# Performance work log

Hardware: AMD Instinct MI355X
Metric: run time of the kernel (lower is better)

The kernel has to match this reference:

```python
import jax, jax.numpy as jnp
import numpy as np

N, E = 50000, 800000
INF, ONF, HNF = 64, 64, 128
EPS = 1e-8


def qmul(p, q):
    # roma XYZW Hamilton product
    px, py, pz, pw = p[:, 0], p[:, 1], p[:, 2], p[:, 3]
    qx, qy, qz, qw = q[:, 0], q[:, 1], q[:, 2], q[:, 3]
    return jnp.stack([
        pw * qx + px * qw + py * qz - pz * qy,
        pw * qy - px * qz + py * qw + pz * qx,
        pw * qz + px * qy - py * qx + pz * qw,
        pw * qw - px * qx - py * qy - pz * qz,
    ], axis=1)


def qinv(q):
    conj = jnp.concatenate([-q[:, :3], q[:, 3:]], axis=1)
    return conj / jnp.sum(q * q, axis=1, keepdims=True)


def rot_apply(q, v):
    # rotate v by unit quaternion q (XYZW)
    qv, w = q[:, :3], q[:, 3:4]
    t = 2.0 * jnp.cross(qv, v)
    return v + w * t + jnp.cross(qv, t)


def quat_exponential(im):
    r = jnp.linalg.norm(im, axis=1, keepdims=True)
    u = im / r
    return jnp.concatenate([u * jnp.sin(r), jnp.cos(r)], axis=1)


def seg_sum(data, ids, n):
    return jax.ops.segment_sum(data, ids, num_segments=n)


def seg_mean(data, ids, n):
    s = seg_sum(data, ids, n)
    c = seg_sum(jnp.ones_like(data), ids, n)
    return s / jnp.maximum(c, 1.0)


def setup_inputs() -> dict:
    key = jax.random.key(0)
    ks = jax.random.split(key, 24)
    h = jax.random.normal(ks[0], (N, INF), jnp.float32)
    coord = jax.random.normal(ks[1], (N, 3), jnp.float32)
    q = jax.random.normal(ks[2], (N, 4), jnp.float32)
    quat = q / jnp.linalg.norm(q, axis=1, keepdims=True)
    edge_index = jax.random.randint(ks[3], (2, E), 0, N)

    def lin(k, fi, fo, scale=None):
        s = (1.0 / np.sqrt(fi)) if scale is None else scale
        return jax.random.uniform(k, (fi, fo), jnp.float32, -s, s)

    ein = 2 * INF + 8  # source, target, radial(1), quat_prod(4), unit_vecs(3)
    params = dict(
        We1=lin(ks[4], ein, HNF), be1=jnp.zeros((HNF,), jnp.float32),
        We2=lin(ks[5], HNF, HNF), be2=jnp.zeros((HNF,), jnp.float32),
        Wn1=lin(ks[6], HNF + INF, HNF), bn1=jnp.zeros((HNF,), jnp.float32),
        Wn2=lin(ks[7], HNF, ONF), bn2=jnp.zeros((ONF,), jnp.float32),
        Wc1=lin(ks[8], HNF, HNF), bc1=jnp.zeros((HNF,), jnp.float32),
        wc2=lin(ks[9], HNF, 1, scale=0.001),  # xavier gain 0.001, no bias
        Wq1=lin(ks[10], HNF, HNF), bq1=jnp.zeros((HNF,), jnp.float32),
        Wq2=lin(ks[11], HNF, 3), bq2=jnp.zeros((3,), jnp.float32),
    )
    return dict(h=h, edge_index=edge_index, coord=coord, quat=quat, **params)


def reference(h, edge_index, coord, quat,
              We1, be1, We2, be2, Wn1, bn1, Wn2, bn2,
              Wc1, bc1, wc2, Wq1, bq1, Wq2, bq2):
    silu = jax.nn.silu
    row, col = edge_index[0], edge_index[1]

    # invariants
    coord_diff = coord[row] - coord[col]                       # [E,3]
    qi = qinv(quat)
    quat_prod = qmul(qi[row], quat[col])                       # [E,4]
    radial = jnp.sum(coord_diff ** 2, axis=1, keepdims=True)   # [E,1]
    norm = jnp.sqrt(radial) + EPS
    unit_vecs = -rot_apply(qi[row], coord_diff / norm)         # [E,3]

    # edge model
    ein = jnp.concatenate([h[row], h[col], radial, quat_prod, unit_vecs], axis=1)
    edge_feat = silu(silu(ein @ We1 + be1) @ We2 + be2)        # [E,HNF]

    # coord model (mean agg)
    trans = coord_diff * (silu(edge_feat @ Wc1 + bc1) @ wc2)   # [E,3]
    coord = coord + seg_mean(trans, row, N)

    # quat model (mean agg)
    tan_vecs = silu(edge_feat @ Wq1 + bq1) @ Wq2 + bq2         # [E,3]
    rots = quat_exponential(seg_mean(tan_vecs, row, N))
    quat = qmul(quat, rots)

    # node model (sum agg), residual
    agg = seg_sum(edge_feat, row, N)
    nin = jnp.concatenate([h, agg], axis=1)
    h = h + (silu(nin @ Wn1 + bn1) @ Wn2 + bn2)
    return (h, coord, quat)
```

## Files before the change

### kernel.cpp

```cpp
#include <hip/hip_runtime.h>
#include <hip/hip_bf16.h>
#include <math.h>


#define N_NODES 50000
#define N_EDGES 800000
#define ASTR 172
#define NSTR 204

typedef __attribute__((ext_vector_type(4))) float f32x4;
typedef __attribute__((ext_vector_type(8))) short bf16x8;
typedef __attribute__((ext_vector_type(4))) unsigned short u16x4;
typedef __attribute__((ext_vector_type(8))) unsigned short u16x8;

static __device__ __forceinline__ unsigned short f2bf(float f) {
  return __builtin_bit_cast(unsigned short, __float2bfloat16(f));
}
static __device__ __forceinline__ float bf2f(unsigned short s) {
  unsigned int u = ((unsigned int)s) << 16;
  return __builtin_bit_cast(float, u);
}
static __device__ __forceinline__ float silu_f(float x) {
  return x * __builtin_amdgcn_rcpf(1.0f + __expf(-x));
}
static __device__ __forceinline__ void atomic_pk_add_bf16(unsigned int* addr,
                                                          float lo, float hi) {
  const unsigned int pk = ((unsigned int)f2bf(hi) << 16) | (unsigned int)f2bf(lo);
  asm volatile("global_atomic_pk_add_bf16 %0, %1, off"
               :: "v"((unsigned long long)(uintptr_t)addr), "v"(pk)
               : "memory");
}

static __device__ __forceinline__ void swz_do(const float* __restrict__ src,
                                              unsigned short* __restrict__ dst,
                                              int K, int NOUT, int NCT, int idx) {
  int lane = idx & 63, blk = idx >> 6;
  int ct = blk % NCT, kt = blk / NCT;
  int col = ct * 16 + (lane & 15);
  int kb = kt * 32 + (lane >> 4) * 8;
  u16x8 o;
  #pragma unroll
  for (int j = 0; j < 8; ++j) {
    int k = kb + j;
    o[j] = (k < K) ? f2bf(src[(size_t)k * NOUT + col]) : (unsigned short)0;
  }
  *(u16x8*)(dst + (size_t)idx * 8) = o;
}

__global__ __launch_bounds__(256) void prep1_kernel(
    const float* __restrict__ We1, const float* __restrict__ We2,
    const float* __restrict__ Wc1, const float* __restrict__ Wq1,
    const float* __restrict__ Wn1, const float* __restrict__ Wn2,
    unsigned short* __restrict__ We1b, unsigned short* __restrict__ We2b,
    unsigned short* __restrict__ Wc1b, unsigned short* __restrict__ Wq1b,
    unsigned short* __restrict__ Wn1b, unsigned short* __restrict__ Wn2b,
    const int* __restrict__ ei, int* __restrict__ cursor)
{
  const int b = blockIdx.x, t = threadIdx.x;
  if (b >= 50) {
    const int e = (b - 50) * 256 + t;
    if (e < N_EDGES) atomicAdd(&cursor[ei[e]], 1);
    return;
  }
  if (b < 10)       swz_do(We1, We1b, 136, 128, 8, b*256 + t);
  else if (b < 18)  swz_do(We2, We2b, 128, 128, 8, (b-10)*256 + t);
  else if (b < 26)  swz_do(Wc1, Wc1b, 128, 128, 8, (b-18)*256 + t);
  else if (b < 34)  swz_do(Wq1, Wq1b, 128, 128, 8, (b-26)*256 + t);
  else if (b < 46) { int i = (b-34)*256 + t; if (i < 3072) swz_do(Wn1, Wn1b, 192, 128, 8, i); }
  else              swz_do(Wn2, Wn2b, 128, 64, 4, (b-46)*256 + t);
}

__global__ void scan_kernel(int* __restrict__ cursor) {
  __shared__ int s[1024];
  const int t = threadIdx.x;
  const int C = 49;
  const int base = t * C;
  int sum = 0;
  for (int i = 0; i < C; ++i) {
    int n = base + i;
    if (n < N_NODES) sum += cursor[n];
  }
  s[t] = sum;
  __syncthreads();
  for (int d = 1; d < 1024; d <<= 1) {
    int v = (t >= d) ? s[t - d] : 0;
    __syncthreads();
    s[t] += v;
    __syncthreads();
  }
  int run = s[t] - sum;
  for (int i = 0; i < C; ++i) {
    int n = base + i;
    if (n < N_NODES) {
      int d = cursor[n];
      cursor[n] = run;
      run += d;
    }
  }
}

__global__ void scatter_kernel(const int* __restrict__ ei, int* __restrict__ cursor,
                               int2* __restrict__ rc2) {
  int e = blockIdx.x * blockDim.x + threadIdx.x;
  if (e < N_EDGES) {
    int r = ei[e];
    int pos = atomicAdd(&cursor[r], 1);
    int2 v; v.x = r; v.y = ei[N_EDGES + e];
    rc2[pos] = v;
  }
}

template <int KT, int NCT>
static __device__ __forceinline__ void mmW2(const unsigned short* __restrict__ a0,
                                            const unsigned short* __restrict__ a1,
                                            int lk,
                                            const unsigned short* __restrict__ Wb,
                                            int lane, f32x4* acc0, f32x4* acc1) {
  const f32x4 zero = {0.f, 0.f, 0.f, 0.f};
  #pragma unroll
  for (int ct = 0; ct < NCT; ++ct) { acc0[ct] = zero; acc1[ct] = zero; }
  __builtin_amdgcn_s_setprio(1);
  #pragma unroll
  for (int kt = 0; kt < KT; ++kt) {
    bf16x8 x0 = *(const bf16x8*)(a0 + kt*32 + lk*8);
    bf16x8 x1 = *(const bf16x8*)(a1 + kt*32 + lk*8);
    const u16x8* bb = (const u16x8*)Wb + (size_t)(kt*NCT)*64 + lane;
    #pragma unroll
    for (int ct = 0; ct < NCT; ++ct) {
      bf16x8 w = *(const bf16x8*)(bb + (size_t)ct*64);
      acc0[ct] = __builtin_amdgcn_mfma_f32_16x16x32_bf16(w, x0, acc0[ct], 0, 0, 0);
      acc1[ct] = __builtin_amdgcn_mfma_f32_16x16x32_bf16(w, x1, acc1[ct], 0, 0, 0);
    }
  }
  __builtin_amdgcn_s_setprio(0);
}

__global__ __launch_bounds__(128, 3) void edge_kernel(
    const float* __restrict__ h,
    const float* __restrict__ coord, const float* __restrict__ quat,
    const int2* __restrict__ rc2,
    const unsigned short* __restrict__ We1b, const unsigned short* __restrict__ We2b,
    const unsigned short* __restrict__ Wc1b, const unsigned short* __restrict__ Wq1b,
    const float* __restrict__ be1, const float* __restrict__ be2,
    const float* __restrict__ bc1, const float* __restrict__ wc2,
    const float* __restrict__ bq1, const float* __restrict__ Wq2,
    const float* __restrict__ bq2,
    unsigned int* __restrict__ agg32, float* __restrict__ transS,
    float* __restrict__ tanS, float* __restrict__ cnt)
{
  __shared__ __align__(16) unsigned short AF[64 * ASTR];

  const int tid = threadIdx.x;
  const int wv = tid >> 6, lane = tid & 63;
  const int lr = lane & 15, lk = lane >> 4;
  const int row0 = wv*32 + lr, row1 = row0 + 16;

  const int xcd = blockIdx.x & 7, idx = blockIdx.x >> 3;
  const int q = 1562, rem = 4;
  const int bid = (xcd < rem ? xcd*(q+1) : rem*(q+1) + (xcd-rem)*q) + idx;
  const int e0 = bid * 64;

  const int2 p0v = rc2[e0 + row0];
  const int2 p1v = rc2[e0 + row1];
  const int r0 = p0v.x, c0 = p0v.y, r1 = p1v.x, c1 = p1v.y;

  {
    const float* hs0 = h + (size_t)(lk < 2 ? r0 : c0) * 64 + (lk & 1) * 32;
    const float* hs1 = h + (size_t)(lk < 2 ? r1 : c1) * 64 + (lk & 1) * 32;
    const int cb = lk * 32;
    #pragma unroll
    for (int j = 0; j < 32; j += 4) {
      f32x4 v0 = *(const f32x4*)(hs0 + j);
      f32x4 v1 = *(const f32x4*)(hs1 + j);
      u16x4 q0, q1;
      #pragma unroll
      for (int i = 0; i < 4; ++i) { q0[i] = f2bf(v0[i]); q1[i] = f2bf(v1[i]); }
      *(u16x4*)&AF[row0*ASTR + cb + j] = q0;
      *(u16x4*)&AF[row1*ASTR + cb + j] = q1;
    }
  }
  const float cdx0 = coord[r0*3+0] - coord[c0*3+0];
  const float cdy0 = coord[r0*3+1] - coord[c0*3+1];
  const float cdz0 = coord[r0*3+2] - coord[c0*3+2];
  const float cdx1 = coord[r1*3+0] - coord[c1*3+0];
  const float cdy1 = coord[r1*3+1] - coord[c1*3+1];
  const float cdz1 = coord[r1*3+2] - coord[c1*3+2];
  if (lk < 2) {
    const int gr = lk ? r1 : r0, gc = lk ? c1 : c0, grow = lk ? row1 : row0;
    const float gx = lk ? cdx1 : cdx0, gy = lk ? cdy1 : cdy0, gz = lk ? cdz1 : cdz0;
    const float radial = gx*gx + gy*gy + gz*gz;
    const float nrm = sqrtf(radial) + 1e-8f;
    const f32x4 qr4 = *(const f32x4*)&quat[gr*4];
    const f32x4 qc4 = *(const f32x4*)&quat[gc*4];
    const float qix = -qr4[0], qiy = -qr4[1], qiz = -qr4[2], qiw = qr4[3];
    const float qcx = qc4[0], qcy = qc4[1], qcz = qc4[2], qcw = qc4[3];
    const float qpx = qiw*qcx + qix*qcw + qiy*qcz - qiz*qcy;
    const float qpy = qiw*qcy - qix*qcz + qiy*qcw + qiz*qcx;
    const float qpz = qiw*qcz + qix*qcy - qiy*qcx + qiz*qcw;
    const float qpw = qiw*qcw - qix*qcx - qiy*qcy - qiz*qcz;
    const float rinv = __builtin_amdgcn_rcpf(nrm);
    const float vx = gx*rinv, vy = gy*rinv, vz = gz*rinv;
    const float tx = 2.f*(qiy*vz - qiz*vy);
    const float ty = 2.f*(qiz*vx - qix*vz);
    const float tz = 2.f*(qix*vy - qiy*vx);
    const float ux = -(vx + qiw*tx + (qiy*tz - qiz*ty));
    const float uy = -(vy + qiw*ty + (qiz*tx - qix*tz));
    const float uz = -(vz + qiw*tz + (qix*ty - qiy*tx));
    u16x4 f0, f1;
    f0[0] = f2bf(radial); f0[1] = f2bf(qpx); f0[2] = f2bf(qpy); f0[3] = f2bf(qpz);
    f1[0] = f2bf(qpw);    f1[1] = f2bf(ux);  f1[2] = f2bf(uy);  f1[3] = f2bf(uz);
    *(u16x4*)&AF[grow*ASTR + 128] = f0;
    *(u16x4*)&AF[grow*ASTR + 132] = f1;
    const u16x4 z4 = {0, 0, 0, 0};
    #pragma unroll
    for (int j = 136; j < 160; j += 4) *(u16x4*)&AF[grow*ASTR + j] = z4;
  }

  f32x4 acc0[8], acc1[8];

  mmW2<5,8>(AF + row0*ASTR, AF + row1*ASTR, lk, We1b, lane, acc0, acc1);
  #pragma unroll
  for (int ct = 0; ct < 8; ++ct) {
    const int ocb = ct*16 + lk*4;
    const f32x4 b4 = *(const f32x4*)&be1[ocb];
    u16x4 k0, k1;
    #pragma unroll
    for (int i = 0; i < 4; ++i) {
      k0[i] = f2bf(silu_f(acc0[ct][i] + b4[i]));
      k1[i] = f2bf(silu_f(acc1[ct][i] + b4[i]));
    }
    *(u16x4*)&AF[row0*ASTR + ocb] = k0;
    *(u16x4*)&AF[row1*ASTR + ocb] = k1;
  }

  mmW2<4,8>(AF + row0*ASTR, AF + row1*ASTR, lk, We2b, lane, acc0, acc1);
  #pragma unroll
  for (int ct = 0; ct < 8; ++ct) {
    const int ocb = ct*16 + lk*4;
    const f32x4 b4 = *(const f32x4*)&be2[ocb];
    u16x4 k0, k1;
    #pragma unroll
    for (int i = 0; i < 4; ++i) {
      k0[i] = f2bf(silu_f(acc0[ct][i] + b4[i]));
      k1[i] = f2bf(silu_f(acc1[ct][i] + b4[i]));
    }
    *(u16x4*)&AF[row0*ASTR + ocb] = k0;
    *(u16x4*)&AF[row1*ASTR + ocb] = k1;
  }

  float pcs0 = 0.f, pcs1 = 0.f;
  mmW2<4,8>(AF + row0*ASTR, AF + row1*ASTR, lk, Wc1b, lane, acc0, acc1);
  #pragma unroll
  for (int ct = 0; ct < 8; ++ct) {
    const int ocb = ct*16 + lk*4;
    const f32x4 b4 = *(const f32x4*)&bc1[ocb];
    const f32x4 w4 = *(const f32x4*)&wc2[ocb];
    #pragma unroll
    for (int i = 0; i < 4; ++i) {
      pcs0 += silu_f(acc0[ct][i] + b4[i]) * w4[i];
      pcs1 += silu_f(acc1[ct][i] + b4[i]) * w4[i];
    }
  }
  pcs0 += __shfl_xor(pcs0, 16);  pcs0 += __shfl_xor(pcs0, 32);
  pcs1 += __shfl_xor(pcs1, 16);  pcs1 += __shfl_xor(pcs1, 32);

  float p00 = 0.f, p10 = 0.f, p20 = 0.f;
  float p01 = 0.f, p11 = 0.f, p21 = 0.f;
  mmW2<4,8>(AF + row0*ASTR, AF + row1*ASTR, lk, Wq1b, lane, acc0, acc1);
  #pragma unroll
  for (int ct = 0; ct < 8; ++ct) {
    const int ocb = ct*16 + lk*4;
    const f32x4 b4 = *(const f32x4*)&bq1[ocb];
    const float* wq = &Wq2[ocb*3];
    const f32x4 qa = *(const f32x4*)(wq);
    const f32x4 qb = *(const f32x4*)(wq + 4);
    const f32x4 qc = *(const f32x4*)(wq + 8);
    {
      const float v0 = silu_f(acc0[ct][0] + b4[0]);
      const float v1 = silu_f(acc0[ct][1] + b4[1]);
      const float v2 = silu_f(acc0[ct][2] + b4[2]);
      const float v3 = silu_f(acc0[ct][3] + b4[3]);
      p00 += v0*qa[0] + v1*qa[3] + v2*qb[2] + v3*qc[1];
      p10 += v0*qa[1] + v1*qb[0] + v2*qb[3] + v3*qc[2];
      p20 += v0*qa[2] + v1*qb[1] + v2*qc[0] + v3*qc[3];
    }
    {
      const float v0 = silu_f(acc1[ct][0] + b4[0]);
      const float v1 = silu_f(acc1[ct][1] + b4[1]);
      const float v2 = silu_f(acc1[ct][2] + b4[2]);
      const float v3 = silu_f(acc1[ct][3] + b4[3]);
      p01 += v0*qa[0] + v1*qa[3] + v2*qb[2] + v3*qc[1];
      p11 += v0*qa[1] + v1*qb[0] + v2*qb[3] + v3*qc[2];
      p21 += v0*qa[2] + v1*qb[1] + v2*qc[0] + v3*qc[3];
    }
  }
  p00 += __shfl_xor(p00, 16);  p00 += __shfl_xor(p00, 32);
  p10 += __shfl_xor(p10, 16);  p10 += __shfl_xor(p10, 32);
  p20 += __shfl_xor(p20, 16);  p20 += __shfl_xor(p20, 32);
  p01 += __shfl_xor(p01, 16);  p01 += __shfl_xor(p01, 32);
  p11 += __shfl_xor(p11, 16);  p11 += __shfl_xor(p11, 32);
  p21 += __shfl_xor(p21, 16);  p21 += __shfl_xor(p21, 32);

  #pragma unroll
  for (int g = 0; g < 2; ++g) {
    const int rg = g ? r1 : r0;
    const int rUp = __shfl_up(rg, 1, 16);
    const int rDn = __shfl_down(rg, 1, 16);
    const bool head = (lr == 0) || (rUp != rg);
    const bool tail = (lr == 15) || (rDn != rg);
    float v1, v2;
    if (lk == 3) { v1 = 1.0f; v2 = 0.f; }
    else {
      const float cdj = (lk == 0) ? (g ? cdx1 : cdx0)
                      : (lk == 1) ? (g ? cdy1 : cdy0) : (g ? cdz1 : cdz0);
      const float pj  = (lk == 0) ? (g ? p01 : p00)
                      : (lk == 1) ? (g ? p11 : p10) : (g ? p21 : p20);
      v1 = cdj * (g ? pcs1 : pcs0);
      v2 = pj + bq2[lk];
    }
    int f = head ? 1 : 0;
    #pragma unroll
    for (int d = 1; d < 16; d <<= 1) {
      const float o1 = __shfl_up(v1, d, 16);
      const float o2 = __shfl_up(v2, d, 16);
      const int   of = __shfl_up(f,  d, 16);
      if (lr >= d) {
        if (!f) { v1 += o1; v2 += o2; }
        f |= of;
      }
    }
    if (tail) {
      if (lk == 3) {
        atomicAdd(&cnt[rg], v1);
      } else {
        atomicAdd(&transS[rg*3 + lk], v1);
        atomicAdd(&tanS[rg*3 + lk], v2);
      }
    }
  }

  {
    float rl_ = 0.f, rh_ = 0.f;
    int prev = __builtin_amdgcn_readlane(r0, 0);
    #pragma unroll
    for (int k2 = 0; k2 < 32; ++k2) {
      const int rr = (k2 < 16) ? __builtin_amdgcn_readlane(r0, k2)
                               : __builtin_amdgcn_readlane(r1, k2 - 16);
      if (rr != prev) {
        atomic_pk_add_bf16(&agg32[(size_t)prev*64 + lane], rl_, rh_);
        rl_ = 0.f; rh_ = 0.f; prev = rr;
      }
      const unsigned int u = *(const unsigned int*)&AF[(wv*32 + k2)*ASTR + 2*lane];
      rl_ += bf2f((unsigned short)(u & 0xffffu));
      rh_ += bf2f((unsigned short)(u >> 16));
    }
    atomic_pk_add_bf16(&agg32[(size_t)prev*64 + lane], rl_, rh_);
  }
}

__global__ __launch_bounds__(256, 4) void node_kernel(
    const float* __restrict__ h, const float* __restrict__ coord,
    const float* __restrict__ quat,
    const unsigned short* __restrict__ aggb, const float* __restrict__ transS,
    const float* __restrict__ tanS, const float* __restrict__ cnt,
    const unsigned short* __restrict__ Wn1b, const unsigned short* __restrict__ Wn2b,
    const float* __restrict__ bn1, const float* __restrict__ bn2,
    float* __restrict__ out_h, float* __restrict__ out_c, float* __restrict__ out_q)
{
  __shared__ unsigned short A_[64][NSTR];
  const int tid = threadIdx.x;
  const int n0 = blockIdx.x * 64;

  {
    const int row = tid >> 2, sub = tid & 3;
    const int n = n0 + row;
    if (n < N_NODES) {
      if (sub < 2) {
        const float* hp = h + (size_t)n*64 + sub*32;
        #pragma unroll
        for (int j = 0; j < 32; j += 4) {
          f32x4 v = *(const f32x4*)(hp + j);
          u16x4 p;
          p[0] = f2bf(v[0]); p[1] = f2bf(v[1]); p[2] = f2bf(v[2]); p[3] = f2bf(v[3]);
          *(u16x4*)&A_[row][sub*32 + j] = p;
        }
      } else {
        const unsigned short* ap = aggb + (size_t)n*128 + (sub - 2)*64;
        #pragma unroll
        for (int j = 0; j < 64; j += 8)
          *(u16x8*)&A_[row][64 + (sub - 2)*64 + j] = *(const u16x8*)(ap + j);
      }
    } else {
      const u16x4 z4 = {0, 0, 0, 0};
      if (sub < 2) {
        #pragma unroll
        for (int j = 0; j < 32; j += 4) *(u16x4*)&A_[row][sub*32 + j] = z4;
      } else {
        #pragma unroll
        for (int j = 0; j < 64; j += 4) *(u16x4*)&A_[row][64 + (sub - 2)*64 + j] = z4;
      }
    }
  }
  __syncthreads();

  const int wv = tid >> 6, lane = tid & 63;
  const int lr = lane & 15, lk = lane >> 4;
  const int nrow = wv*16 + lr;
  f32x4 acc[8];

  {
    const f32x4 zero = {0.f, 0.f, 0.f, 0.f};
    #pragma unroll
    for (int ct = 0; ct < 8; ++ct) acc[ct] = zero;
    #pragma unroll
    for (int kt = 0; kt < 6; ++kt) {
      bf16x8 act = *(const bf16x8*)&A_[nrow][kt*32 + lk*8];
      const u16x8* bb = (const u16x8*)Wn1b + (size_t)(kt*8)*64 + lane;
      #pragma unroll
      for (int ct = 0; ct < 8; ++ct) {
        bf16x8 w = *(const bf16x8*)(bb + (size_t)ct*64);
        acc[ct] = __builtin_amdgcn_mfma_f32_16x16x32_bf16(w, act, acc[ct], 0, 0, 0);
      }
    }
  }
  #pragma unroll
  for (int ct = 0; ct < 8; ++ct) {
    const int ocb = ct*16 + lk*4;
    const f32x4 b4 = *(const f32x4*)&bn1[ocb];
    u16x4 pk;
    #pragma unroll
    for (int i = 0; i < 4; ++i) pk[i] = f2bf(silu_f(acc[ct][i] + b4[i]));
    *(u16x4*)&A_[nrow][ocb] = pk;
  }

  f32x4 acc2[4];
  {
    const f32x4 zero = {0.f, 0.f, 0.f, 0.f};
    #pragma unroll
    for (int ct = 0; ct < 4; ++ct) acc2[ct] = zero;
    #pragma unroll
    for (int kt = 0; kt < 4; ++kt) {
      bf16x8 act = *(const bf16x8*)&A_[nrow][kt*32 + lk*8];
      const u16x8* bb = (const u16x8*)Wn2b + (size_t)(kt*4)*64 + lane;
      #pragma unroll
      for (int ct = 0; ct < 4; ++ct) {
        bf16x8 w = *(const bf16x8*)(bb + (size_t)ct*64);
        acc2[ct] = __builtin_amdgcn_mfma_f32_16x16x32_bf16(w, act, acc2[ct], 0, 0, 0);
      }
    }
  }
  const int n = n0 + nrow;
  if (n < N_NODES) {
    #pragma unroll
    for (int ct = 0; ct < 4; ++ct) {
      const int ocb = ct*16 + lk*4;
      const f32x4 b4 = *(const f32x4*)&bn2[ocb];
      const f32x4 h4 = *(const f32x4*)&h[(size_t)n*64 + ocb];
      f32x4 o;
      #pragma unroll
      for (int i = 0; i < 4; ++i) o[i] = h4[i] + acc2[ct][i] + b4[i];
      *(f32x4*)&out_h[(size_t)n*64 + ocb] = o;
    }
  }

  if (tid < 64) {
    const int nn = n0 + tid;
    if (nn < N_NODES) {
      const float cm = fmaxf(cnt[nn], 1.0f);
      const float inv = 1.0f / cm;
      out_c[nn*3+0] = coord[nn*3+0] + transS[nn*3+0]*inv;
      out_c[nn*3+1] = coord[nn*3+1] + transS[nn*3+1]*inv;
      out_c[nn*3+2] = coord[nn*3+2] + transS[nn*3+2]*inv;
      const float ix = tanS[nn*3+0]*inv, iy = tanS[nn*3+1]*inv, iz = tanS[nn*3+2]*inv;
      const float rr = sqrtf(ix*ix + iy*iy + iz*iz);
      const float s = sinf(rr) / rr;
      const float rx = ix*s, ry = iy*s, rz = iz*s, rw = cosf(rr);
      const float px = quat[nn*4+0], py = quat[nn*4+1], pz = quat[nn*4+2], pw = quat[nn*4+3];
      out_q[nn*4+0] = pw*rx + px*rw + py*rz - pz*ry;
      out_q[nn*4+1] = pw*ry - px*rz + py*rw + pz*rx;
      out_q[nn*4+2] = pw*rz + px*ry - py*rx + pz*rw;
      out_q[nn*4+3] = pw*rw - px*rx - py*ry - pz*rz;
    }
  }
}

extern "C" void kernel_launch(void* const* d_in, const int* in_sizes, int n_in,
                              void* d_out, int out_size, void* d_ws, size_t ws_size,
                              hipStream_t stream) {
  (void)in_sizes; (void)n_in; (void)out_size; (void)ws_size;
  const float* h     = (const float*)d_in[0];
  const int*   ei    = (const int*)d_in[1];
  const float* coord = (const float*)d_in[2];
  const float* quat  = (const float*)d_in[3];
  const float* We1 = (const float*)d_in[4];  const float* be1 = (const float*)d_in[5];
  const float* We2 = (const float*)d_in[6];  const float* be2 = (const float*)d_in[7];
  const float* Wn1 = (const float*)d_in[8];  const float* bn1 = (const float*)d_in[9];
  const float* Wn2 = (const float*)d_in[10]; const float* bn2 = (const float*)d_in[11];
  const float* Wc1 = (const float*)d_in[12]; const float* bc1 = (const float*)d_in[13];
  const float* wc2 = (const float*)d_in[14];
  const float* Wq1 = (const float*)d_in[15]; const float* bq1 = (const float*)d_in[16];
  const float* Wq2 = (const float*)d_in[17]; const float* bq2 = (const float*)d_in[18];

  char* ws = (char*)d_ws;
  unsigned int* agg32  = (unsigned int*)(ws);
  unsigned short* aggb = (unsigned short*)(ws);
  float* transS = (float*)(ws + 12800000);
  float* tanS   = (float*)(ws + 13400000);
  float* cnt    = (float*)(ws + 14000000);
  int*   cursor = (int*)  (ws + 14200000);
  int2*  rc2    = (int2*) (ws + 14600064);
  unsigned short* We1b = (unsigned short*)(ws + 21000064);
  unsigned short* We2b = We1b + 5*8*64*8;
  unsigned short* Wc1b = We2b + 4*8*64*8;
  unsigned short* Wq1b = Wc1b + 4*8*64*8;
  unsigned short* Wn1b = Wq1b + 4*8*64*8;
  unsigned short* Wn2b = Wn1b + 6*8*64*8;

  hipMemsetAsync(ws, 0, 14400000, stream);
  prep1_kernel<<<50 + (N_EDGES + 255)/256, 256, 0, stream>>>(
      We1, We2, Wc1, Wq1, Wn1, Wn2, We1b, We2b, Wc1b, Wq1b, Wn1b, Wn2b,
      ei, cursor);
  scan_kernel<<<1, 1024, 0, stream>>>(cursor);
  scatter_kernel<<<(N_EDGES + 255)/256, 256, 0, stream>>>(ei, cursor, rc2);

  edge_kernel<<<N_EDGES/64, 128, 0, stream>>>(
      h, coord, quat, rc2, We1b, We2b, Wc1b, Wq1b,
      be1, be2, bc1, wc2, bq1, Wq2, bq2, agg32, transS, tanS, cnt);

  float* out_h = (float*)d_out;
  float* out_c = out_h + (size_t)N_NODES*64;
  float* out_q = out_c + (size_t)N_NODES*3;
  node_kernel<<<(N_NODES + 63)/64, 256, 0, stream>>>(
      h, coord, quat, aggb, transS, tanS, cnt, Wn1b, Wn2b, bn1, bn2,
      out_h, out_c, out_q);
}
```

Before: 477.2 us.

## Pre-convert h to bf16, fold biases into MFMA init, derive degree from CSR

The prep kernel now converts h to bf16 once, and both the edge and node kernels gather those bf16 rows. This halves the bytes read by the per-edge random gathers and removes the repeated per-edge conversion. The prep kernel also zeroes the aggregation buffers, so the large memset shrinks to clearing only the cursor array. Biases are loaded into the MFMA accumulators at the start instead of being added later. The per-edge count atomics are dropped, and the node kernel computes each node's degree from the CSR cursor offsets instead. The cost is an extra pass over h and more blocks in the prep launch.

```diff
diff --git a/kernel.cpp b/kernel.cpp
--- a/kernel.cpp
+++ b/kernel.cpp
@@ -51,23 +51,42 @@
     const float* __restrict__ We1, const float* __restrict__ We2,
     const float* __restrict__ Wc1, const float* __restrict__ Wq1,
     const float* __restrict__ Wn1, const float* __restrict__ Wn2,
+    const float* __restrict__ h,
     unsigned short* __restrict__ We1b, unsigned short* __restrict__ We2b,
     unsigned short* __restrict__ Wc1b, unsigned short* __restrict__ Wq1b,
     unsigned short* __restrict__ Wn1b, unsigned short* __restrict__ Wn2b,
+    unsigned short* __restrict__ hb, uint4* __restrict__ zbase,
     const int* __restrict__ ei, int* __restrict__ cursor)
 {
   const int b = blockIdx.x, t = threadIdx.x;
-  if (b >= 50) {
-    const int e = (b - 50) * 256 + t;
-    if (e < N_EDGES) atomicAdd(&cursor[ei[e]], 1);
+  if (b < 50) {
+    if (b < 10)       swz_do(We1, We1b, 136, 128, 8, b*256 + t);
+    else if (b < 18)  swz_do(We2, We2b, 128, 128, 8, (b-10)*256 + t);
+    else if (b < 26)  swz_do(Wc1, Wc1b, 128, 128, 8, (b-18)*256 + t);
+    else if (b < 34)  swz_do(Wq1, Wq1b, 128, 128, 8, (b-26)*256 + t);
+    else if (b < 46) { int i = (b-34)*256 + t; if (i < 3072) swz_do(Wn1, Wn1b, 192, 128, 8, i); }
+    else              swz_do(Wn2, Wn2b, 128, 64, 4, (b-46)*256 + t);
     return;
   }
-  if (b < 10)       swz_do(We1, We1b, 136, 128, 8, b*256 + t);
-  else if (b < 18)  swz_do(We2, We2b, 128, 128, 8, (b-10)*256 + t);
-  else if (b < 26)  swz_do(Wc1, Wc1b, 128, 128, 8, (b-18)*256 + t);
-  else if (b < 34)  swz_do(Wq1, Wq1b, 128, 128, 8, (b-26)*256 + t);
-  else if (b < 46) { int i = (b-34)*256 + t; if (i < 3072) swz_do(Wn1, Wn1b, 192, 128, 8, i); }
-  else              swz_do(Wn2, Wn2b, 128, 64, 4, (b-46)*256 + t);
+  if (b < 1613) {
+    const int i8 = (b - 50) * 2048 + t * 8;
+    if (i8 < N_NODES * 64) {
+      f32x4 v0 = *(const f32x4*)(h + i8);
+      f32x4 v1 = *(const f32x4*)(h + i8 + 4);
+      u16x8 o;
+      #pragma unroll
+      for (int i = 0; i < 4; ++i) { o[i] = f2bf(v0[i]); o[i+4] = f2bf(v1[i]); }
+      *(u16x8*)(hb + i8) = o;
+    }
+    return;
+  }
+  if (b < 5031) {
+    const int i = (b - 1613) * 256 + t;
+    if (i < 875000) { uint4 z; z.x = z.y = z.z = z.w = 0u; zbase[i] = z; }
+    return;
+  }
+  const int e = (b - 5031) * 256 + t;
+  if (e < N_EDGES) atomicAdd(&cursor[ei[e]], 1);
 }
 
 __global__ void scan_kernel(int* __restrict__ cursor) {
@@ -115,10 +134,13 @@
                                             const unsigned short* __restrict__ a1,
                                             int lk,
                                             const unsigned short* __restrict__ Wb,
+                                            const float* __restrict__ bias,
                                             int lane, f32x4* acc0, f32x4* acc1) {
-  const f32x4 zero = {0.f, 0.f, 0.f, 0.f};
-  #pragma unroll
-  for (int ct = 0; ct < NCT; ++ct) { acc0[ct] = zero; acc1[ct] = zero; }
+  #pragma unroll
+  for (int ct = 0; ct < NCT; ++ct) {
+    const f32x4 b = *(const f32x4*)&bias[ct*16 + lk*4];
+    acc0[ct] = b; acc1[ct] = b;
+  }
   __builtin_amdgcn_s_setprio(1);
   #pragma unroll
   for (int kt = 0; kt < KT; ++kt) {
@@ -136,7 +158,7 @@
 }
 
 __global__ __launch_bounds__(128, 3) void edge_kernel(
-    const float* __restrict__ h,
+    const unsigned short* __restrict__ hb,
     const float* __restrict__ coord, const float* __restrict__ quat,
     const int2* __restrict__ rc2,
     const unsigned short* __restrict__ We1b, const unsigned short* __restrict__ We2b,
@@ -146,7 +168,7 @@
     const float* __restrict__ bq1, const float* __restrict__ Wq2,
     const float* __restrict__ bq2,
     unsigned int* __restrict__ agg32, float* __restrict__ transS,
-    float* __restrict__ tanS, float* __restrict__ cnt)
+    float* __restrict__ tanS)
 {
   __shared__ __align__(16) unsigned short AF[64 * ASTR];
 
@@ -165,18 +187,13 @@
   const int r0 = p0v.x, c0 = p0v.y, r1 = p1v.x, c1 = p1v.y;
 
   {
-    const float* hs0 = h + (size_t)(lk < 2 ? r0 : c0) * 64 + (lk & 1) * 32;
-    const float* hs1 = h + (size_t)(lk < 2 ? r1 : c1) * 64 + (lk & 1) * 32;
+    const unsigned short* hs0 = hb + (size_t)(lk < 2 ? r0 : c0) * 64 + (lk & 1) * 32;
+    const unsigned short* hs1 = hb + (size_t)(lk < 2 ? r1 : c1) * 64 + (lk & 1) * 32;
     const int cb = lk * 32;
     #pragma unroll
     for (int j = 0; j < 32; j += 4) {
-      f32x4 v0 = *(const f32x4*)(hs0 + j);
-      f32x4 v1 = *(const f32x4*)(hs1 + j);
-      u16x4 q0, q1;
-      #pragma unroll
-      for (int i = 0; i < 4; ++i) { q0[i] = f2bf(v0[i]); q1[i] = f2bf(v1[i]); }
-      *(u16x4*)&AF[row0*ASTR + cb + j] = q0;
-      *(u16x4*)&AF[row1*ASTR + cb + j] = q1;
+      *(u16x4*)&AF[row0*ASTR + cb + j] = *(const u16x4*)(hs0 + j);
+      *(u16x4*)&AF[row1*ASTR + cb + j] = *(const u16x4*)(hs1 + j);
     }
   }
   const float cdx0 = coord[r0*3+0] - coord[c0*3+0];
@@ -218,47 +235,44 @@
 
   f32x4 acc0[8], acc1[8];
 
-  mmW2<5,8>(AF + row0*ASTR, AF + row1*ASTR, lk, We1b, lane, acc0, acc1);
+  mmW2<5,8>(AF + row0*ASTR, AF + row1*ASTR, lk, We1b, be1, lane, acc0, acc1);
   #pragma unroll
   for (int ct = 0; ct < 8; ++ct) {
     const int ocb = ct*16 + lk*4;
-    const f32x4 b4 = *(const f32x4*)&be1[ocb];
     u16x4 k0, k1;
     #pragma unroll
     for (int i = 0; i < 4; ++i) {
-      k0[i] = f2bf(silu_f(acc0[ct][i] + b4[i]));
-      k1[i] = f2bf(silu_f(acc1[ct][i] + b4[i]));
+      k0[i] = f2bf(silu_f(acc0[ct][i]));
+      k1[i] = f2bf(silu_f(acc1[ct][i]));
     }
     *(u16x4*)&AF[row0*ASTR + ocb] = k0;
     *(u16x4*)&AF[row1*ASTR + ocb] = k1;
   }
 
-  mmW2<4,8>(AF + row0*ASTR, AF + row1*ASTR, lk, We2b, lane, acc0, acc1);
+  mmW2<4,8>(AF + row0*ASTR, AF + row1*ASTR, lk, We2b, be2, lane, acc0, acc1);
   #pragma unroll
   for (int ct = 0; ct < 8; ++ct) {
     const int ocb = ct*16 + lk*4;
-    const f32x4 b4 = *(const f32x4*)&be2[ocb];
     u16x4 k0, k1;
     #pragma unroll
     for (int i = 0; i < 4; ++i) {
-      k0[i] = f2bf(silu_f(acc0[ct][i] + b4[i]));
-      k1[i] = f2bf(silu_f(acc1[ct][i] + b4[i]));
+      k0[i] = f2bf(silu_f(acc0[ct][i]));
+      k1[i] = f2bf(silu_f(acc1[ct][i]));
     }
     *(u16x4*)&AF[row0*ASTR + ocb] = k0;
     *(u16x4*)&AF[row1*ASTR + ocb] = k1;
   }
 
   float pcs0 = 0.f, pcs1 = 0.f;
-  mmW2<4,8>(AF + row0*ASTR, AF + row1*ASTR, lk, Wc1b, lane, acc0, acc1);
+  mmW2<4,8>(AF + row0*ASTR, AF + row1*ASTR, lk, Wc1b, bc1, lane, acc0, acc1);
   #pragma unroll
   for (int ct = 0; ct < 8; ++ct) {
     const int ocb = ct*16 + lk*4;
-    const f32x4 b4 = *(const f32x4*)&bc1[ocb];
     const f32x4 w4 = *(const f32x4*)&wc2[ocb];
     #pragma unroll
     for (int i = 0; i < 4; ++i) {
-      pcs0 += silu_f(acc0[ct][i] + b4[i]) * w4[i];
-      pcs1 += silu_f(acc1[ct][i] + b4[i]) * w4[i];
+      pcs0 += silu_f(acc0[ct][i]) * w4[i];
+      pcs1 += silu_f(acc1[ct][i]) * w4[i];
     }
   }
   pcs0 += __shfl_xor(pcs0, 16);  pcs0 += __shfl_xor(pcs0, 32);
@@ -266,29 +280,28 @@
 
   float p00 = 0.f, p10 = 0.f, p20 = 0.f;
   float p01 = 0.f, p11 = 0.f, p21 = 0.f;
-  mmW2<4,8>(AF + row0*ASTR, AF + row1*ASTR, lk, Wq1b, lane, acc0, acc1);
+  mmW2<4,8>(AF + row0*ASTR, AF + row1*ASTR, lk, Wq1b, bq1, lane, acc0, acc1);
   #pragma unroll
   for (int ct = 0; ct < 8; ++ct) {
     const int ocb = ct*16 + lk*4;
-    const f32x4 b4 = *(const f32x4*)&bq1[ocb];
     const float* wq = &Wq2[ocb*3];
     const f32x4 qa = *(const f32x4*)(wq);
     const f32x4 qb = *(const f32x4*)(wq + 4);
     const f32x4 qc = *(const f32x4*)(wq + 8);
     {
-      const float v0 = silu_f(acc0[ct][0] + b4[0]);
-      const float v1 = silu_f(acc0[ct][1] + b4[1]);
-      const float v2 = silu_f(acc0[ct][2] + b4[2]);
-      const float v3 = silu_f(acc0[ct][3] + b4[3]);
+      const float v0 = silu_f(acc0[ct][0]);
+      const float v1 = silu_f(acc0[ct][1]);
+      const float v2 = silu_f(acc0[ct][2]);
+      const float v3 = silu_f(acc0[ct][3]);
       p00 += v0*qa[0] + v1*qa[3] + v2*qb[2] + v3*qc[1];
       p10 += v0*qa[1] + v1*qb[0] + v2*qb[3] + v3*qc[2];
       p20 += v0*qa[2] + v1*qb[1] + v2*qc[0] + v3*qc[3];
     }
     {
-      const float v0 = silu_f(acc1[ct][0] + b4[0]);
-      const float v1 = silu_f(acc1[ct][1] + b4[1]);
-      const float v2 = silu_f(acc1[ct][2] + b4[2]);
-      const float v3 = silu_f(acc1[ct][3] + b4[3]);
+      const float v0 = silu_f(acc1[ct][0]);
+      const float v1 = silu_f(acc1[ct][1]);
+      const float v2 = silu_f(acc1[ct][2]);
+      const float v3 = silu_f(acc1[ct][3]);
       p01 += v0*qa[0] + v1*qa[3] + v2*qb[2] + v3*qc[1];
       p11 += v0*qa[1] + v1*qb[0] + v2*qb[3] + v3*qc[2];
       p21 += v0*qa[2] + v1*qb[1] + v2*qc[0] + v3*qc[3];
@@ -301,38 +314,32 @@
   p11 += __shfl_xor(p11, 16);  p11 += __shfl_xor(p11, 32);
   p21 += __shfl_xor(p21, 16);  p21 += __shfl_xor(p21, 32);
 
-  #pragma unroll
-  for (int g = 0; g < 2; ++g) {
-    const int rg = g ? r1 : r0;
-    const int rUp = __shfl_up(rg, 1, 16);
-    const int rDn = __shfl_down(rg, 1, 16);
-    const bool head = (lr == 0) || (rUp != rg);
-    const bool tail = (lr == 15) || (rDn != rg);
-    float v1, v2;
-    if (lk == 3) { v1 = 1.0f; v2 = 0.f; }
-    else {
+  if (lk < 3) {
+    #pragma unroll
+    for (int g = 0; g < 2; ++g) {
+      const int rg = g ? r1 : r0;
+      const int rUp = __shfl_up(rg, 1, 16);
+      const int rDn = __shfl_down(rg, 1, 16);
+      const bool head = (lr == 0) || (rUp != rg);
+      const bool tail = (lr == 15) || (rDn != rg);
       const float cdj = (lk == 0) ? (g ? cdx1 : cdx0)
                       : (lk == 1) ? (g ? cdy1 : cdy0) : (g ? cdz1 : cdz0);
       const float pj  = (lk == 0) ? (g ? p01 : p00)
                       : (lk == 1) ? (g ? p11 : p10) : (g ? p21 : p20);
-      v1 = cdj * (g ? pcs1 : pcs0);
-      v2 = pj + bq2[lk];
-    }
-    int f = head ? 1 : 0;
-    #pragma unroll
-    for (int d = 1; d < 16; d <<= 1) {
-      const float o1 = __shfl_up(v1, d, 16);
-      const float o2 = __shfl_up(v2, d, 16);
-      const int   of = __shfl_up(f,  d, 16);
-      if (lr >= d) {
-        if (!f) { v1 += o1; v2 += o2; }
-        f |= of;
-      }
-    }
-    if (tail) {
-      if (lk == 3) {
-        atomicAdd(&cnt[rg], v1);
-      } else {
+      float v1 = cdj * (g ? pcs1 : pcs0);
+      float v2 = pj + bq2[lk];
+      int f = head ? 1 : 0;
+      #pragma unroll
+      for (int d = 1; d < 16; d <<= 1) {
+        const float o1 = __shfl_up(v1, d, 16);
+        const float o2 = __shfl_up(v2, d, 16);
+        const int   of = __shfl_up(f,  d, 16);
+        if (lr >= d) {
+          if (!f) { v1 += o1; v2 += o2; }
+          f |= of;
+        }
+      }
+      if (tail) {
         atomicAdd(&transS[rg*3 + lk], v1);
         atomicAdd(&tanS[rg*3 + lk], v2);
       }
@@ -359,10 +366,10 @@
 }
 
 __global__ __launch_bounds__(256, 4) void node_kernel(
-    const float* __restrict__ h, const float* __restrict__ coord,
-    const float* __restrict__ quat,
+    const float* __restrict__ h, const unsigned short* __restrict__ hb,
+    const float* __restrict__ coord, const float* __restrict__ quat,
     const unsigned short* __restrict__ aggb, const float* __restrict__ transS,
-    const float* __restrict__ tanS, const float* __restrict__ cnt,
+    const float* __restrict__ tanS, const int* __restrict__ cursor,
     const unsigned short* __restrict__ Wn1b, const unsigned short* __restrict__ Wn2b,
     const float* __restrict__ bn1, const float* __restrict__ bn2,
     float* __restrict__ out_h, float* __restrict__ out_c, float* __restrict__ out_q)
@@ -376,14 +383,10 @@
     const int n = n0 + row;
     if (n < N_NODES) {
       if (sub < 2) {
-        const float* hp = h + (size_t)n*64 + sub*32;
+        const unsigned short* hp = hb + (size_t)n*64 + sub*32;
         #pragma unroll
-        for (int j = 0; j < 32; j += 4) {
-          f32x4 v = *(const f32x4*)(hp + j);
-          u16x4 p;
-          p[0] = f2bf(v[0]); p[1] = f2bf(v[1]); p[2] = f2bf(v[2]); p[3] = f2bf(v[3]);
-          *(u16x4*)&A_[row][sub*32 + j] = p;
-        }
+        for (int j = 0; j < 32; j += 4)
+          *(u16x4*)&A_[row][sub*32 + j] = *(const u16x4*)(hp + j);
       } else {
         const unsigned short* ap = aggb + (size_t)n*128 + (sub - 2)*64;
         #pragma unroll
@@ -409,9 +412,9 @@
   f32x4 acc[8];
 
   {
-    const f32x4 zero = {0.f, 0.f, 0.f, 0.f};
-    #pragma unroll
-    for (int ct = 0; ct < 8; ++ct) acc[ct] = zero;
+    #pragma unroll
+    for (int ct = 0; ct < 8; ++ct)
+      acc[ct] = *(const f32x4*)&bn1[ct*16 + lk*4];
     #pragma unroll
     for (int kt = 0; kt < 6; ++kt) {
       bf16x8 act = *(const bf16x8*)&A_[nrow][kt*32 + lk*8];
@@ -426,18 +429,17 @@
   #pragma unroll
   for (int ct = 0; ct < 8; ++ct) {
     const int ocb = ct*16 + lk*4;
-    const f32x4 b4 = *(const f32x4*)&bn1[ocb];
     u16x4 pk;
     #pragma unroll
-    for (int i = 0; i < 4; ++i) pk[i] = f2bf(silu_f(acc[ct][i] + b4[i]));
+    for (int i = 0; i < 4; ++i) pk[i] = f2bf(silu_f(acc[ct][i]));
     *(u16x4*)&A_[nrow][ocb] = pk;
   }
 
   f32x4 acc2[4];
   {
-    const f32x4 zero = {0.f, 0.f, 0.f, 0.f};
-    #pragma unroll
-    for (int ct = 0; ct < 4; ++ct) acc2[ct] = zero;
+    #pragma unroll
+    for (int ct = 0; ct < 4; ++ct)
+      acc2[ct] = *(const f32x4*)&bn2[ct*16 + lk*4];
     #pragma unroll
     for (int kt = 0; kt < 4; ++kt) {
       bf16x8 act = *(const bf16x8*)&A_[nrow][kt*32 + lk*8];
@@ -454,11 +456,10 @@
     #pragma unroll
     for (int ct = 0; ct < 4; ++ct) {
       const int ocb = ct*16 + lk*4;
-      const f32x4 b4 = *(const f32x4*)&bn2[ocb];
       const f32x4 h4 = *(const f32x4*)&h[(size_t)n*64 + ocb];
       f32x4 o;
       #pragma unroll
-      for (int i = 0; i < 4; ++i) o[i] = h4[i] + acc2[ct][i] + b4[i];
+      for (int i = 0; i < 4; ++i) o[i] = h4[i] + acc2[ct][i];
       *(f32x4*)&out_h[(size_t)n*64 + ocb] = o;
     }
   }
@@ -466,8 +467,8 @@
   if (tid < 64) {
     const int nn = n0 + tid;
     if (nn < N_NODES) {
-      const float cm = fmaxf(cnt[nn], 1.0f);
-      const float inv = 1.0f / cm;
+      const int deg = cursor[nn] - (nn ? cursor[nn-1] : 0);
+      const float inv = 1.0f / fmaxf((float)deg, 1.0f);
       out_c[nn*3+0] = coord[nn*3+0] + transS[nn*3+0]*inv;
       out_c[nn*3+1] = coord[nn*3+1] + transS[nn*3+1]*inv;
       out_c[nn*3+2] = coord[nn*3+2] + transS[nn*3+2]*inv;
@@ -506,7 +507,6 @@
   unsigned short* aggb = (unsigned short*)(ws);
   float* transS = (float*)(ws + 12800000);
   float* tanS   = (float*)(ws + 13400000);
-  float* cnt    = (float*)(ws + 14000000);
   int*   cursor = (int*)  (ws + 14200000);
   int2*  rc2    = (int2*) (ws + 14600064);
   unsigned short* We1b = (unsigned short*)(ws + 21000064);
@@ -515,22 +515,23 @@
   unsigned short* Wq1b = Wc1b + 4*8*64*8;
   unsigned short* Wn1b = Wq1b + 4*8*64*8;
   unsigned short* Wn2b = Wn1b + 6*8*64*8;
-
-  hipMemsetAsync(ws, 0, 14400000, stream);
-  prep1_kernel<<<50 + (N_EDGES + 255)/256, 256, 0, stream>>>(
-      We1, We2, Wc1, Wq1, Wn1, Wn2, We1b, We2b, Wc1b, Wq1b, Wn1b, Wn2b,
-      ei, cursor);
+  unsigned short* hb   = (unsigned short*)(ws + 21204864);
+
+  hipMemsetAsync(cursor, 0, 200000, stream);
+  prep1_kernel<<<8156, 256, 0, stream>>>(
+      We1, We2, Wc1, Wq1, Wn1, Wn2, h,
+      We1b, We2b, Wc1b, Wq1b, Wn1b, Wn2b, hb, (uint4*)ws, ei, cursor);
   scan_kernel<<<1, 1024, 0, stream>>>(cursor);
   scatter_kernel<<<(N_EDGES + 255)/256, 256, 0, stream>>>(ei, cursor, rc2);
 
   edge_kernel<<<N_EDGES/64, 128, 0, stream>>>(
-      h, coord, quat, rc2, We1b, We2b, Wc1b, Wq1b,
-      be1, be2, bc1, wc2, bq1, Wq2, bq2, agg32, transS, tanS, cnt);
+      hb, coord, quat, rc2, We1b, We2b, Wc1b, Wq1b,
+      be1, be2, bc1, wc2, bq1, Wq2, bq2, agg32, transS, tanS);
 
   float* out_h = (float*)d_out;
   float* out_c = out_h + (size_t)N_NODES*64;
   float* out_q = out_c + (size_t)N_NODES*3;
   node_kernel<<<(N_NODES + 63)/64, 256, 0, stream>>>(
-      h, coord, quat, aggb, transS, tanS, cnt, Wn1b, Wn2b, bn1, bn2,
+      h, hb, coord, quat, aggb, transS, tanS, cursor, Wn1b, Wn2b, bn1, bn2,
       out_h, out_c, out_q);
 }
```

Measured after the change: 459.1 us. 3.8% less time.
